# Optimization experiments

Hardware: AMD Instinct MI355X
Metric: run time of the kernel (lower is better)

## Reference

```python
import jax, jax.numpy as jnp
import numpy as np

SCALE, R_MAX, ALPHA = 16, 8, 2.0
HL, WL, C_FEAT = 16, 16, 384
HH, WH = HL * SCALE, WL * SCALE


def bilinear_resize(img, out_h, out_w):
    """PyTorch F.interpolate(mode='bilinear', align_corners=False, antialias=False).
    img: [..., H, W] -> [..., out_h, out_w]."""
    H, W = img.shape[-2], img.shape[-1]
    ys = jnp.maximum((jnp.arange(out_h, dtype=jnp.float32) + 0.5) * (H / out_h) - 0.5, 0.0)
    xs = jnp.maximum((jnp.arange(out_w, dtype=jnp.float32) + 0.5) * (W / out_w) - 0.5, 0.0)
    y0 = jnp.floor(ys).astype(jnp.int32)
    x0 = jnp.floor(xs).astype(jnp.int32)
    y1 = jnp.minimum(y0 + 1, H - 1)
    x1 = jnp.minimum(x0 + 1, W - 1)
    wy = (ys - y0)[:, None]
    wx = (xs - x0)[None, :]
    g = lambda yi, xi: img[..., yi[:, None], xi[None, :]]
    return ((1 - wy) * (1 - wx) * g(y0, x0) + (1 - wy) * wx * g(y0, x1)
            + wy * (1 - wx) * g(y1, x0) + wy * wx * g(y1, x1))


def jbu_forward(feat_lr, guide_hr, sx_raw, sy_raw, th_raw, sr_raw):
    C, Hl, Wl = feat_lr.shape[1], feat_lr.shape[2], feat_lr.shape[3]
    Hh, Wh = guide_hr.shape[2], guide_hr.shape[3]
    scale, R_max, alpha = SCALE, R_MAX, ALPHA
    NEG = -1e30  # finite stand-in for -inf (keeps grads NaN-free)

    # parameter transforms from the module
    sx = jnp.exp(sx_raw[0, 0])
    sy = jnp.exp(sy_raw[0, 0])
    th = jnp.pi * jnp.tanh(th_raw[0, 0])
    sr = jnp.exp(sr_raw[0, 0])

    Y, X = jnp.meshgrid(jnp.arange(Hh, dtype=jnp.float32),
                        jnp.arange(Wh, dtype=jnp.float32), indexing='ij')
    u = (Y + 0.5) / scale - 0.5
    v = (X + 0.5) / scale - 0.5
    uc = jnp.clip(jnp.round(u), 0, Hl - 1).astype(jnp.int32)
    vc = jnp.clip(jnp.round(v), 0, Wl - 1).astype(jnp.int32)

    sigma_eff_hr = bilinear_resize(jnp.maximum(sx, sy), Hh, Wh)
    R_map = jnp.clip(jnp.ceil(alpha * sigma_eff_hr), 1.0, float(R_max))  # [Hh,Wh]

    offs = jnp.arange(-R_max, R_max + 1, dtype=jnp.int32)
    dYg, dXg = jnp.meshgrid(offs, offs, indexing='ij')
    dY = dYg.reshape(-1)[:, None, None]  # [N,1,1]
    dX = dXg.reshape(-1)[:, None, None]

    Ui = jnp.clip(uc[None] + dY, 0, Hl - 1)  # [N,Hh,Wh]
    Vi = jnp.clip(vc[None] + dX, 0, Wl - 1)
    idx = Ui * Wl + Vi                       # flat LR index per (neighbor, HR pixel)
    gat = lambda mp: mp.reshape(-1)[idx]

    sxg = jnp.maximum(gat(sx), 1e-6)
    syg = jnp.maximum(gat(sy), 1e-6)
    thg = gat(th)
    srg = jnp.maximum(gat(sr), 1e-6)

    dx = X[None] - ((Vi.astype(jnp.float32) + 0.5) * scale - 0.5)
    dyv = Y[None] - ((Ui.astype(jnp.float32) + 0.5) * scale - 0.5)
    ct, st = jnp.cos(thg), jnp.sin(thg)
    a = dx * ct + dyv * st
    b = -dx * st + dyv * ct

    guide_lr = bilinear_resize(guide_hr[0], Hl, Wl)  # [3,Hl,Wl]
    g_diff2 = sum((guide_hr[0, c][None] - gat(guide_lr[c])) ** 2 for c in range(3))

    log_w = (-a * a / (2 * sxg ** 2 + 1e-8)
             - b * b / (2 * syg ** 2 + 1e-8)
             - g_diff2 / (2.0 * srg ** 2 + 1e-8))  # [N,Hh,Wh]

    mask = (dY * dY + dX * dX).astype(jnp.float32) <= R_map[None] ** 2
    log_w = jnp.where(mask, log_w, NEG)

    # numerically stable softmax over neighbors (== online-softmax result)
    m = log_w.max(axis=0)
    s = jnp.exp(log_w - m[None])  # masked entries underflow to 0
    den = s.sum(axis=0)           # [Hh,Wh]

    # num[c,h,w] = sum_n s[n,h,w] * feat[idx[n,h,w], c]
    # scatter neighbor weights by LR pixel, then one GEMM with the LR features
    N = idx.shape[0]
    idx2 = idx.reshape(N, Hh * Wh)
    cols = jnp.arange(Hh * Wh, dtype=jnp.int32)[None, :]
    acc = jnp.zeros((Hl * Wl, Hh * Wh), jnp.float32).at[idx2, cols].add(s.reshape(N, -1))
    feat_flat = feat_lr[0].reshape(C, Hl * Wl)  # [C, P]
    num = jnp.einsum('cp,pq->cq', feat_flat, acc).reshape(C, Hh, Wh)

    return (num / jnp.maximum(den, 1e-8)[None])[None]  # [1,C,Hh,Wh]


def setup_inputs() -> dict:
    key = jax.random.key(0)
    k1, k2, k3, k4, k5, k6 = jax.random.split(key, 6)
    feat_lr = jax.random.normal(k1, (1, C_FEAT, HL, WL), jnp.float32)
    guide_hr = jax.random.uniform(k2, (1, 3, HH, WH), dtype=jnp.float32)
    log_sigma = float(np.log(16.0))
    log_sigma_r = float(np.log(0.12))
    sx_raw = log_sigma + 0.1 * jax.random.normal(k3, (1, 1, HL, WL), jnp.float32)
    sy_raw = log_sigma + 0.1 * jax.random.normal(k4, (1, 1, HL, WL), jnp.float32)
    th_raw = 0.1 * jax.random.normal(k5, (1, 1, HL, WL), jnp.float32)
    sr_raw = log_sigma_r + 0.1 * jax.random.normal(k6, (1, 1, HL, WL), jnp.float32)
    return {"feat_lr": feat_lr, "guide_hr": guide_hr, "sx_raw": sx_raw,
            "sy_raw": sy_raw, "th_raw": th_raw, "sr_raw": sr_raw}


def reference(feat_lr, guide_hr, sx_raw, sy_raw, th_raw, sr_raw):
    return jbu_forward(feat_lr, guide_hr, sx_raw, sy_raw, th_raw, sr_raw)
```

## Files before the change

kernel.cpp:

```cpp
#include <hip/hip_runtime.h>
#include <math.h>

#define NEG_BIG (-1e30f)

typedef _Float16 half8 __attribute__((ext_vector_type(8)));
typedef _Float16 half2v __attribute__((ext_vector_type(2)));
typedef float floatx4 __attribute__((ext_vector_type(4)));

__global__ __launch_bounds__(256) void setup_all(
    const float* __restrict__ feat, const float* __restrict__ guide,
    const float* __restrict__ sx_raw, const float* __restrict__ sy_raw,
    const float* __restrict__ th_raw, const float* __restrict__ sr_raw,
    _Float16* __restrict__ feat16, float4* __restrict__ PQ,
    float4* __restrict__ PG)
{
    const int b = blockIdx.x, t = threadIdx.x;
    if (b < 384) {
        int i = b*256 + t;
        feat16[i] = (_Float16)feat[i];
        return;
    }
    float sx = expf(sx_raw[t]);
    float sy = expf(sy_raw[t]);
    float th = 3.14159265358979323846f * tanhf(th_raw[t]);
    float sr = expf(sr_raw[t]);
    float sxg = fmaxf(sx, 1e-6f), syg = fmaxf(sy, 1e-6f), srg = fmaxf(sr, 1e-6f);
    float iA = 1.f / (2.f*sxg*sxg + 1e-8f);
    float iB = 1.f / (2.f*syg*syg + 1e-8f);
    float iC = 1.f / (2.f*srg*srg + 1e-8f);
    float ct = cosf(th), st = sinf(th);
    float A2 = iA*ct*ct + iB*st*st;
    float B2 = 2.f*ct*st*(iA - iB);
    float C2 = iA*st*st + iB*ct*ct;
    PQ[t] = make_float4(A2, B2, C2, iC);
    int i = t >> 4, j = t & 15;
    int y0 = 16*i + 7, x0 = 16*j + 7;
    float g[3];
#pragma unroll
    for (int c = 0; c < 3; ++c) {
        const float* gp = guide + c*65536;
        g[c] = 0.25f*(gp[y0*256 + x0]     + gp[y0*256 + x0 + 1] +
                      gp[(y0+1)*256 + x0] + gp[(y0+1)*256 + x0 + 1]);
    }
    PG[t] = make_float4(g[0], g[1], g[2], fmaxf(sx, sy));
}

__global__ __launch_bounds__(256, 3) void jbu_main(
    const float* __restrict__ guide, const _Float16* __restrict__ feat16,
    const float4* __restrict__ PQ, const float4* __restrict__ PG,
    float* __restrict__ out)
{
    __shared__ float4 sPQ[256];
    __shared__ float4 sPG[256];
    __shared__ float  LC[4096];
    __shared__ __align__(16) _Float16 Wb[32][256];
    __shared__ float red[8][32];
    __shared__ float invden[32];

    const int t = threadIdx.x;
    sPQ[t] = PQ[t];
    sPG[t] = PG[t];

    const int q   = t & 31;
    const int grp = t >> 5;
    const int Y   = blockIdx.y;
    const int X0  = blockIdx.x << 5;
    const int X   = X0 + q;
    const float Yf = (float)Y, Xf = (float)X;
    const int uc  = Y >> 4;
    const int vc0 = X0 >> 4;

    {
        const int Pu  = t >> 4;
        const int col = t & 15;
        const int Rt  = (col >> 1) + 1;
        const int vcb = col & 1;
        const int vc  = vc0 + vcb;
        const int R2  = Rt * Rt;
        int ylo = (Pu == 0)  ? -8 : (Pu - uc);
        int yhi = (Pu == 15) ?  8 : (Pu - uc);
        ylo = max(ylo, -8); yhi = min(yhi, 8);
        int cnt[16];
#pragma unroll
        for (int Pv = 0; Pv < 16; ++Pv) cnt[Pv] = 0;
        for (int dY = ylo; dY <= yhi; ++dY) {
            int lim = R2 - dY*dY;
            if (lim >= 0) {
                int r = (int)sqrtf((float)lim);
#pragma unroll
                for (int Pv = 0; Pv < 16; ++Pv) {
                    int xlo = (Pv == 0)  ? -8 : (Pv - vc);
                    int xhi = (Pv == 15) ?  8 : (Pv - vc);
                    xlo = max(xlo, -8); xhi = min(xhi, 8);
                    int lo = max(xlo, -r), hi = min(xhi, r);
                    cnt[Pv] += max(0, hi - lo + 1);
                }
            }
        }
#pragma unroll
        for (int Pv = 0; Pv < 16; ++Pv)
            LC[(Pu*16 + Pv)*16 + col] =
                (cnt[Pv] > 0) ? __logf((float)cnt[Pv]) : NEG_BIG;
    }
    __syncthreads();

    float u = (Yf + 0.5f)*0.0625f - 0.5f;
    float v = (Xf + 0.5f)*0.0625f - 0.5f;
    float ysc = fmaxf(u, 0.f), xsc = fmaxf(v, 0.f);
    int y0 = (int)ysc, x0 = (int)xsc;
    int y1 = min(y0 + 1, 15), x1 = min(x0 + 1, 15);
    float wy = ysc - (float)y0, wx = xsc - (float)x0;
    float s00 = sPG[y0*16 + x0].w, s01 = sPG[y0*16 + x1].w;
    float s10 = sPG[y1*16 + x0].w, s11 = sPG[y1*16 + x1].w;
    float sig = (1.f - wy)*((1.f - wx)*s00 + wx*s01)
              +        wy *((1.f - wx)*s10 + wx*s11);
    float Rf = fminf(fmaxf(ceilf(2.f*sig), 1.f), 8.f);
    const int colq = ((int)Rf - 1)*2 + (q >> 4);

    const float g0 = guide[          (Y << 8) + X];
    const float g1 = guide[ 65536 + ((Y << 8) + X)];
    const float g2 = guide[131072 + ((Y << 8) + X)];

    const int pbase = grp << 5;
    const float dy0 = Yf - (16.f*(float)(grp*2) + 7.5f);
    float lw[32];
    float mloc = NEG_BIG;
#pragma unroll
    for (int pi = 0; pi < 32; ++pi) {
        int p = pbase + pi;
        float4 Q = sPQ[p];
        float4 G = sPG[p];
        float dy = (pi < 16) ? dy0 : (dy0 - 16.f);
        float dx = Xf - (16.f*(float)(pi & 15) + 7.5f);
        float d0 = g0 - G.x, d1 = g1 - G.y, d2 = g2 - G.z;
        float gd = d0*d0 + d1*d1 + d2*d2;
        float quad = Q.x*(dx*dx) + Q.y*(dx*dy) + Q.z*(dy*dy) + Q.w*gd;
        float w = LC[p*16 + colq] - quad;
        lw[pi] = w;
        mloc = fmaxf(mloc, w);
    }
    red[grp][q] = mloc;
    __syncthreads();
    float m = red[0][q];
#pragma unroll
    for (int g = 1; g < 8; ++g) m = fmaxf(m, red[g][q]);
    __syncthreads();

    float dloc = 0.f;
#pragma unroll
    for (int pi = 0; pi < 32; pi += 2) {
        int p = pbase + pi;
        float s0 = __expf(lw[pi]     - m);
        float s1 = __expf(lw[pi + 1] - m);
        half2v hh; hh[0] = (_Float16)s0; hh[1] = (_Float16)s1;
        int chunk = ((p >> 3) ^ q) & 31;
        *(half2v*)&Wb[q][chunk*8 + (p & 7)] = hh;
        dloc += (float)hh[0] + (float)hh[1];
    }
    red[grp][q] = dloc;
    __syncthreads();
    float den = 0.f;
#pragma unroll
    for (int g = 0; g < 8; ++g) den += red[g][q];
    if (grp == 0) invden[q] = 1.f / fmaxf(den, 1e-8f);
    __syncthreads();

    const int lane = t & 63;
    const int wv   = t >> 6;
    const int mrow = lane & 15;
    const int quad = lane >> 4;
    const int c0   = wv * 96;

    floatx4 acc[6][2] = {};
    const _Float16* fbase = feat16 + (c0 + mrow)*256 + quad*8;

#pragma unroll
    for (int ks = 0; ks < 8; ++ks) {
        half8 a[6];
#pragma unroll
        for (int mt = 0; mt < 6; ++mt)
            a[mt] = *(const half8*)(fbase + mt*16*256 + ks*32);
        half8 b[2];
#pragma unroll
        for (int nt = 0; nt < 2; ++nt) {
            int pix = nt*16 + mrow;
            int chunk = ((ks*4 + quad) ^ pix) & 31;
            b[nt] = *(const half8*)(&Wb[pix][chunk*8]);
        }
#pragma unroll
        for (int mt = 0; mt < 6; ++mt)
#pragma unroll
            for (int nt = 0; nt < 2; ++nt)
                acc[mt][nt] = __builtin_amdgcn_mfma_f32_16x16x32_f16(
                    a[mt], b[nt], acc[mt][nt], 0, 0, 0);
    }

    const int outbase = (Y << 8) + X0;
#pragma unroll
    for (int nt = 0; nt < 2; ++nt) {
        float idv = invden[nt*16 + mrow];
#pragma unroll
        for (int mt = 0; mt < 6; ++mt) {
            int crow = c0 + mt*16 + quad*4;
            float* o = out + (size_t)crow*65536 + outbase + nt*16 + mrow;
#pragma unroll
            for (int r = 0; r < 4; ++r)
                o[(size_t)r*65536] = acc[mt][nt][r] * idv;
        }
    }
}

extern "C" void kernel_launch(void* const* d_in, const int* in_sizes, int n_in,
                              void* d_out, int out_size, void* d_ws, size_t ws_size,
                              hipStream_t stream)
{
    const float* feat   = (const float*)d_in[0];
    const float* guide  = (const float*)d_in[1];
    const float* sx_raw = (const float*)d_in[2];
    const float* sy_raw = (const float*)d_in[3];
    const float* th_raw = (const float*)d_in[4];
    const float* sr_raw = (const float*)d_in[5];
    float* out = (float*)d_out;

    _Float16* feat16 = (_Float16*)d_ws;
    float4*   PQ     = (float4*)((char*)d_ws + 196608);
    float4*   PG     = (float4*)((char*)d_ws + 196608 + 4096);

    setup_all<<<385, 256, 0, stream>>>(feat, guide, sx_raw, sy_raw, th_raw,
                                       sr_raw, feat16, PQ, PG);
    jbu_main<<<dim3(8, 256), 256, 0, stream>>>(guide, feat16, PQ, PG, out);
}
```

Measured before the change: 166.9 us.

## Shrink LDS, cut barriers, and compute neighbor counts in closed form

Stores the log-count table as fp16 instead of fp32 and raises the launch bound from 3 to 4 blocks per CU, so more blocks fit in the LDS and register budget. The max and denominator reductions now combine the two half-waves with a cross-lane shuffle first, which removes two of the four block barriers and the separate invden array. The count setup replaces the per-row loop over all 16 columns with a closed-form count for the interior columns, looping only for the two edge columns. The risks are the precision loss of fp16 log-counts with a -60000 sentinel, and register spills under the tighter launch bound.

```diff
diff --git a/kernel.cpp b/kernel.cpp
--- a/kernel.cpp
+++ b/kernel.cpp
@@ -1,11 +1,12 @@
 #include <hip/hip_runtime.h>
 #include <math.h>
 
-#define NEG_BIG (-1e30f)
-
-typedef _Float16 half8 __attribute__((ext_vector_type(8)));
+#define NEG_BIG  (-1e30f)
+#define NEG_H16  (-60000.0f)
+
+typedef _Float16 half8  __attribute__((ext_vector_type(8)));
 typedef _Float16 half2v __attribute__((ext_vector_type(2)));
-typedef float floatx4 __attribute__((ext_vector_type(4)));
+typedef float    floatx4 __attribute__((ext_vector_type(4)));
 
 __global__ __launch_bounds__(256) void setup_all(
     const float* __restrict__ feat, const float* __restrict__ guide,
@@ -45,62 +46,77 @@
     PG[t] = make_float4(g[0], g[1], g[2], fmaxf(sx, sy));
 }
 
-__global__ __launch_bounds__(256, 3) void jbu_main(
+__global__ __launch_bounds__(256, 4) void jbu_main(
     const float* __restrict__ guide, const _Float16* __restrict__ feat16,
     const float4* __restrict__ PQ, const float4* __restrict__ PG,
     float* __restrict__ out)
 {
     __shared__ float4 sPQ[256];
     __shared__ float4 sPG[256];
-    __shared__ float  LC[4096];
+    __shared__ _Float16 LCh[4096];
     __shared__ __align__(16) _Float16 Wb[32][256];
-    __shared__ float red[8][32];
-    __shared__ float invden[32];
+    __shared__ float redM[4][32];
+    __shared__ float redD[4][32];
 
     const int t = threadIdx.x;
     sPQ[t] = PQ[t];
     sPG[t] = PG[t];
 
-    const int q   = t & 31;
-    const int grp = t >> 5;
-    const int Y   = blockIdx.y;
-    const int X0  = blockIdx.x << 5;
-    const int X   = X0 + q;
+    const int q    = t & 31;
+    const int grp  = t >> 5;
+    const int wv   = t >> 6;
+    const int Y    = blockIdx.y;
+    const int X0   = blockIdx.x << 5;
+    const int X    = X0 + q;
     const float Yf = (float)Y, Xf = (float)X;
-    const int uc  = Y >> 4;
-    const int vc0 = X0 >> 4;
+    const int uc   = Y >> 4;
+    const int vc0  = X0 >> 4;
 
     {
         const int Pu  = t >> 4;
         const int col = t & 15;
         const int Rt  = (col >> 1) + 1;
-        const int vcb = col & 1;
-        const int vc  = vc0 + vcb;
+        const int vc  = vc0 + (col & 1);
         const int R2  = Rt * Rt;
         int ylo = (Pu == 0)  ? -8 : (Pu - uc);
         int yhi = (Pu == 15) ?  8 : (Pu - uc);
         ylo = max(ylo, -8); yhi = min(yhi, 8);
         int cnt[16];
 #pragma unroll
-        for (int Pv = 0; Pv < 16; ++Pv) cnt[Pv] = 0;
-        for (int dY = ylo; dY <= yhi; ++dY) {
-            int lim = R2 - dY*dY;
-            if (lim >= 0) {
-                int r = (int)sqrtf((float)lim);
-#pragma unroll
-                for (int Pv = 0; Pv < 16; ++Pv) {
-                    int xlo = (Pv == 0)  ? -8 : (Pv - vc);
-                    int xhi = (Pv == 15) ?  8 : (Pv - vc);
-                    xlo = max(xlo, -8); xhi = min(xhi, 8);
-                    int lo = max(xlo, -r), hi = min(xhi, r);
-                    cnt[Pv] += max(0, hi - lo + 1);
+        for (int Pv = 1; Pv < 15; ++Pv) {
+            int d = Pv - vc;
+            int lim = R2 - d*d;
+            int c = 0;
+            if (lim >= 0 && ylo <= yhi) {
+                int s = (int)sqrtf((float)lim);
+                c = max(0, min(yhi, s) - max(ylo, -s) + 1);
+            }
+            cnt[Pv] = c;
+        }
+        cnt[0] = 0;
+        if (-vc >= -8) {
+            for (int dY = ylo; dY <= yhi; ++dY) {
+                int lim = R2 - dY*dY;
+                if (lim >= 0) {
+                    int r = (int)sqrtf((float)lim);
+                    cnt[0] += max(0, min(-vc, r) + r + 1);
                 }
             }
         }
+        cnt[15] = 0;
+        if (15 - vc <= 8) {
+            for (int dY = ylo; dY <= yhi; ++dY) {
+                int lim = R2 - dY*dY;
+                if (lim >= 0) {
+                    int r = (int)sqrtf((float)lim);
+                    cnt[15] += max(0, r - max(15 - vc, -r) + 1);
+                }
+            }
+        }
 #pragma unroll
         for (int Pv = 0; Pv < 16; ++Pv)
-            LC[(Pu*16 + Pv)*16 + col] =
-                (cnt[Pv] > 0) ? __logf((float)cnt[Pv]) : NEG_BIG;
+            LCh[(Pu*16 + Pv)*16 + col] = (_Float16)
+                ((cnt[Pv] > 0) ? __logf((float)cnt[Pv]) : NEG_H16);
     }
     __syncthreads();
 
@@ -135,41 +151,43 @@
         float d0 = g0 - G.x, d1 = g1 - G.y, d2 = g2 - G.z;
         float gd = d0*d0 + d1*d1 + d2*d2;
         float quad = Q.x*(dx*dx) + Q.y*(dx*dy) + Q.z*(dy*dy) + Q.w*gd;
-        float w = LC[p*16 + colq] - quad;
+        float w = (float)LCh[p*16 + colq] - quad;
         lw[pi] = w;
         mloc = fmaxf(mloc, w);
     }
-    red[grp][q] = mloc;
+    mloc = fmaxf(mloc, __shfl_xor(mloc, 32, 64));
+    redM[wv][q] = mloc;
     __syncthreads();
-    float m = red[0][q];
-#pragma unroll
-    for (int g = 1; g < 8; ++g) m = fmaxf(m, red[g][q]);
-    __syncthreads();
+    float m = fmaxf(fmaxf(redM[0][q], redM[1][q]),
+                    fmaxf(redM[2][q], redM[3][q]));
 
     float dloc = 0.f;
 #pragma unroll
     for (int pi = 0; pi < 32; pi += 2) {
         int p = pbase + pi;
-        float s0 = __expf(lw[pi]     - m);
-        float s1 = __expf(lw[pi + 1] - m);
-        half2v hh; hh[0] = (_Float16)s0; hh[1] = (_Float16)s1;
+        float e0 = __expf(lw[pi]     - m);
+        float e1 = __expf(lw[pi + 1] - m);
+        half2v hh; hh[0] = (_Float16)e0; hh[1] = (_Float16)e1;
         int chunk = ((p >> 3) ^ q) & 31;
         *(half2v*)&Wb[q][chunk*8 + (p & 7)] = hh;
         dloc += (float)hh[0] + (float)hh[1];
     }
-    red[grp][q] = dloc;
+    dloc += __shfl_xor(dloc, 32, 64);
+    redD[wv][q] = dloc;
     __syncthreads();
-    float den = 0.f;
-#pragma unroll
-    for (int g = 0; g < 8; ++g) den += red[g][q];
-    if (grp == 0) invden[q] = 1.f / fmaxf(den, 1e-8f);
-    __syncthreads();
 
     const int lane = t & 63;
-    const int wv   = t >> 6;
     const int mrow = lane & 15;
     const int quad = lane >> 4;
     const int c0   = wv * 96;
+
+    float idv[2];
+#pragma unroll
+    for (int nt = 0; nt < 2; ++nt) {
+        int pix = nt*16 + mrow;
+        float den = redD[0][pix] + redD[1][pix] + redD[2][pix] + redD[3][pix];
+        idv[nt] = 1.f / fmaxf(den, 1e-8f);
+    }
 
     floatx4 acc[6][2] = {};
     const _Float16* fbase = feat16 + (c0 + mrow)*256 + quad*8;
@@ -198,14 +216,13 @@
     const int outbase = (Y << 8) + X0;
 #pragma unroll
     for (int nt = 0; nt < 2; ++nt) {
-        float idv = invden[nt*16 + mrow];
 #pragma unroll
         for (int mt = 0; mt < 6; ++mt) {
             int crow = c0 + mt*16 + quad*4;
             float* o = out + (size_t)crow*65536 + outbase + nt*16 + mrow;
 #pragma unroll
             for (int r = 0; r < 4; ++r)
-                o[(size_t)r*65536] = acc[mt][nt][r] * idv;
+                o[(size_t)r*65536] = acc[mt][nt][r] * idv[nt];
         }
     }
 }
```

Result: faster. 162.0 us (-3.0%).
